# Performance work log

Hardware: AMD Instinct MI355X
Metric: run time of the kernel (lower is better)

Reference implementation:

```python
import math
import jax, jax.numpy as jnp
import numpy as np

B, T, D = 8, 2048, 512


def setup_inputs() -> dict:
    key = jax.random.key(0)
    kx, = jax.random.split(key, 1)
    x = jax.random.normal(kx, (B, T, D), dtype=jnp.float32)
    log_tau = jnp.asarray(math.log(2.0), dtype=jnp.float32)
    log_blend = jnp.asarray(math.log(0.3 / 0.7), dtype=jnp.float32)
    return {"x": x, "log_tau": log_tau, "log_blend": log_blend}


def _gelu_tanh(x):
    c = math.sqrt(2.0 / math.pi)
    return 0.5 * x * (1.0 + jnp.tanh(c * (x + 0.044715 * x * x * x)))


def reference(x, log_tau, log_blend):
    Bb, Tt, Dd = x.shape
    tau = jnp.exp(log_tau)
    alpha = jax.nn.sigmoid(log_blend)
    # F.normalize(x, dim=-1): divide by L2 norm clamped to eps=1e-12
    norm = jnp.maximum(jnp.linalg.norm(x, axis=-1, keepdims=True), 1e-12)
    x_norm = x / norm
    # cosine self-similarity [B, T, T]
    sim = jnp.einsum("btd,bsd->bts", x_norm, x_norm)
    # triu(diagonal=0) masks j >= i (current + future positions)
    causal_mask = jnp.triu(jnp.ones((Tt, Tt), dtype=bool), k=0)
    sim_causal = jnp.where(causal_mask[None, :, :], -jnp.inf, sim)
    max_sim = jnp.max(sim_causal, axis=-1)  # [B, T]; row 0 is -inf
    max_sim = jnp.nan_to_num(max_sim, nan=0.0, posinf=1.0, neginf=-1.0)
    novelty = jnp.exp(-tau * max_sim)
    scale = (1.0 - alpha + alpha * novelty)[..., None]  # [B, T, 1]
    return _gelu_tanh(x * scale)
```

## Files before the change

kernel.cpp:

```cpp
#include <hip/hip_runtime.h>

#define B_ 8
#define T_ 2048
#define D_ 512
#define BT 128
#define BK 64
#define NT (T_/BT)
#define NTILES (NT*(NT+1)/2)
#define KTILES (D_/BK)

typedef float f32x4 __attribute__((ext_vector_type(4)));
typedef __bf16 bf16x8 __attribute__((ext_vector_type(8)));

__device__ __forceinline__ unsigned encf(float f) {
    int i = __float_as_int(f);
    return (i < 0) ? ~((unsigned)i) : (((unsigned)i) | 0x80000000u);
}
__device__ __forceinline__ float decf(unsigned u) {
    unsigned b = (u & 0x80000000u) ? (u ^ 0x80000000u) : ~u;
    return __int_as_float((int)b);
}

__device__ __forceinline__ void gload_lds16(const __bf16* g, __bf16* l) {
    __builtin_amdgcn_global_load_lds(
        (const __attribute__((address_space(1))) unsigned int*)g,
        (__attribute__((address_space(3))) unsigned int*)l, 16, 0, 0);
}

__global__ __launch_bounds__(256) void rownorm_kernel(
        const float* __restrict__ x, __bf16* __restrict__ xn,
        unsigned* __restrict__ msim) {
    int row  = blockIdx.x * 4 + (threadIdx.x >> 6);
    int lane = threadIdx.x & 63;
    const float* p = x + (size_t)row * D_ + lane * 8;
    float4 a = *(const float4*)p;
    float4 b = *(const float4*)(p + 4);
    float ss = a.x*a.x + a.y*a.y + a.z*a.z + a.w*a.w
             + b.x*b.x + b.y*b.y + b.z*b.z + b.w*b.w;
#pragma unroll
    for (int m = 32; m; m >>= 1) ss += __shfl_xor(ss, m);
    float r = 1.0f / fmaxf(sqrtf(ss), 1e-12f);
    bf16x8 h;
    h[0] = (__bf16)(a.x * r); h[1] = (__bf16)(a.y * r);
    h[2] = (__bf16)(a.z * r); h[3] = (__bf16)(a.w * r);
    h[4] = (__bf16)(b.x * r); h[5] = (__bf16)(b.y * r);
    h[6] = (__bf16)(b.z * r); h[7] = (__bf16)(b.w * r);
    *(bf16x8*)(xn + (size_t)row * D_ + lane * 8) = h;
    if (lane == 0) msim[row] = 0x407FFFFFu;
}

__global__ __launch_bounds__(256, 2) void simmax_kernel(
        const __bf16* __restrict__ xn, unsigned* __restrict__ msim) {
    __shared__ __attribute__((aligned(16))) __bf16 sA[2][BT * BK];
    __shared__ __attribute__((aligned(16))) __bf16 sB[2][BT * BK];

    int bid = blockIdx.x;
    int b   = bid & 7;
    int s   = bid >> 3;
    int it  = 0;
    while ((it + 1) * (it + 2) / 2 <= s) it++;
    int jt  = s - it * (it + 1) / 2;
    const bool diag = (it == jt);

    int tid  = threadIdx.x;
    int lane = tid & 63;
    int w    = tid >> 6;
    int wr   = w >> 1;
    int wc   = w & 1;
    int fr   = lane & 15;
    int kg   = lane >> 4;

    const size_t rowA0 = (size_t)b * T_ + (size_t)it * BT;
    const size_t rowB0 = (size_t)b * T_ + (size_t)jt * BT;

    int rb   = lane >> 3;
    int csrc = (lane & 7) ^ rb;
    const __bf16* gA = xn + (rowA0 + w * 8 + rb) * D_ + csrc * 8;
    const __bf16* gB = xn + (rowB0 + w * 8 + rb) * D_ + csrc * 8;

    f32x4 acc[4][4];
#pragma unroll
    for (int m = 0; m < 4; m++)
#pragma unroll
        for (int n = 0; n < 4; n++)
            acc[m][n] = (f32x4){0.f, 0.f, 0.f, 0.f};

    int swz = (fr & 7) << 4;
    int laA = (wr * 64 + fr) * 128 + kg * 16;
    int laB = (wc * 64 + fr) * 128 + kg * 16;

#define STAGE_A(buf, kc) do {                                              \
    _Pragma("unroll")                                                      \
    for (int p = 0; p < 4; p++)                                            \
        gload_lds16(gA + (size_t)p * 32 * D_ + (kc) * BK,                  \
                    &sA[buf][(p * 32 + w * 8) * BK]);                      \
} while (0)
#define STAGE_B(buf, kc) do {                                              \
    _Pragma("unroll")                                                      \
    for (int p = 0; p < 4; p++)                                            \
        gload_lds16(gB + (size_t)p * 32 * D_ + (kc) * BK,                  \
                    &sB[buf][(p * 32 + w * 8) * BK]);                      \
} while (0)

    STAGE_A(0, 0);
    if (!diag) STAGE_B(0, 0);

    for (int kc = 0; kc < KTILES; kc++) {
        int cur = kc & 1, nxt = cur ^ 1;
        if (kc < KTILES - 1) {
            STAGE_A(nxt, kc + 1);
            asm volatile("s_waitcnt vmcnt(4)" ::: "memory");
        } else {
            asm volatile("s_waitcnt vmcnt(0)" ::: "memory");
        }
        __builtin_amdgcn_sched_barrier(0);
        asm volatile("s_barrier" ::: "memory");
        __builtin_amdgcn_sched_barrier(0);

        const char* bA = (const char*)&sA[cur][0];
        const char* bB = diag ? (const char*)&sA[cur][0]
                              : (const char*)&sB[cur][0];

        bf16x8 af[4][2], b0[2][2];
#pragma unroll
        for (int m = 0; m < 4; m++)
#pragma unroll
            for (int ks = 0; ks < 2; ks++)
                af[m][ks] = *(const bf16x8*)(bA +
                              ((laA + m * 2048 + ks * 64) ^ swz));
#pragma unroll
        for (int n = 0; n < 2; n++)
#pragma unroll
            for (int ks = 0; ks < 2; ks++)
                b0[n][ks] = *(const bf16x8*)(bB +
                              ((laB + n * 2048 + ks * 64) ^ swz));
        asm volatile("s_waitcnt lgkmcnt(0)" ::: "memory");
        __builtin_amdgcn_sched_barrier(0);
        __builtin_amdgcn_s_setprio(1);
#pragma unroll
        for (int m = 0; m < 4; m++)
#pragma unroll
            for (int n = 0; n < 2; n++)
#pragma unroll
                for (int ks = 0; ks < 2; ks++)
                    acc[m][n] = __builtin_amdgcn_mfma_f32_16x16x32_bf16(
                        af[m][ks], b0[n][ks], acc[m][n], 0, 0, 0);
        __builtin_amdgcn_s_setprio(0);
        __builtin_amdgcn_sched_barrier(0);

        if (kc < KTILES - 1 && !diag) STAGE_B(nxt, kc + 1);

        bf16x8 b1[2][2];
#pragma unroll
        for (int n = 0; n < 2; n++)
#pragma unroll
            for (int ks = 0; ks < 2; ks++)
                b1[n][ks] = *(const bf16x8*)(bB +
                              ((laB + (n + 2) * 2048 + ks * 64) ^ swz));
        asm volatile("s_waitcnt lgkmcnt(0)" ::: "memory");
        __builtin_amdgcn_sched_barrier(0);
        __builtin_amdgcn_s_setprio(1);
#pragma unroll
        for (int m = 0; m < 4; m++)
#pragma unroll
            for (int n = 0; n < 2; n++)
#pragma unroll
                for (int ks = 0; ks < 2; ks++)
                    acc[m][n + 2] = __builtin_amdgcn_mfma_f32_16x16x32_bf16(
                        af[m][ks], b1[n][ks], acc[m][n + 2], 0, 0, 0);
        __builtin_amdgcn_s_setprio(0);
        __builtin_amdgcn_sched_barrier(0);
    }
#undef STAGE_A
#undef STAGE_B

    unsigned* mrow = msim + (size_t)b * T_ + (size_t)it * BT;
    const float NINF = -__builtin_inff();
#pragma unroll
    for (int m = 0; m < 4; m++) {
#pragma unroll
        for (int e = 0; e < 4; e++) {
            int rloc = wr * 64 + m * 16 + kg * 4 + e;
            float v = NINF;
#pragma unroll
            for (int n = 0; n < 4; n++) {
                int cloc = wc * 64 + n * 16 + fr;
                float t = acc[m][n][e];
                if (diag && cloc >= rloc) t = NINF;
                v = fmaxf(v, t);
            }
            v = fmaxf(v, __shfl_xor(v, 1));
            v = fmaxf(v, __shfl_xor(v, 2));
            v = fmaxf(v, __shfl_xor(v, 4));
            v = fmaxf(v, __shfl_xor(v, 8));
            if (fr == 0) atomicMax(&mrow[rloc], encf(v));
        }
    }
}

__global__ __launch_bounds__(256) void gelu_kernel(
        const float* __restrict__ x, const unsigned* __restrict__ msim,
        const float* __restrict__ ltau, const float* __restrict__ lblend,
        float* __restrict__ out) {
    int i = blockIdx.x * 256 + threadIdx.x;
    float tau   = __expf(ltau[0]);
    float alpha = 1.f / (1.f + __expf(-lblend[0]));
    int row = i >> 7;
    float ms = decf(msim[row]);
    float sc = (1.f - alpha) + alpha * __expf(-tau * ms);
    float4 v = ((const float4*)x)[i];
    const float c0 = 0.7978845608028654f;
    const float c1 = 0.044715f;
    float4 o;
#pragma unroll
    for (int j = 0; j < 4; j++) {
        float z = ((const float*)&v)[j] * sc;
        float u = c0 * (z + c1 * z * z * z);
        float t = __expf(2.f * u);
        float th = 1.f - 2.f / (t + 1.f);
        ((float*)&o)[j] = 0.5f * z * (1.f + th);
    }
    ((float4*)out)[i] = o;
}

extern "C" void kernel_launch(void* const* d_in, const int* in_sizes, int n_in,
                              void* d_out, int out_size, void* d_ws, size_t ws_size,
                              hipStream_t stream) {
    (void)in_sizes; (void)n_in; (void)out_size; (void)ws_size;
    const float* x      = (const float*)d_in[0];
    const float* ltau   = (const float*)d_in[1];
    const float* lblend = (const float*)d_in[2];
    float*    out   = (float*)d_out;
    __bf16*   xn    = (__bf16*)d_out;
    unsigned* msim  = (unsigned*)d_ws;

    rownorm_kernel<<<B_ * T_ / 4, 256, 0, stream>>>(x, xn, msim);
    simmax_kernel<<<B_ * NTILES, 256, 0, stream>>>(xn, msim);
    gelu_kernel<<<(B_ * T_ * D_ / 4) / 256, 256, 0, stream>>>(x, msim, ltau, lblend, out);
}
```

Baseline: 63.35 us.

## Use 256x256 off-diagonal tiles with 512-thread blocks and small diagonal tiles

The causal similarity-max kernel now covers strictly-lower off-diagonal 256x256 blocks with 8-wave, 512-thread workgroups, and handles the diagonal band with 128x128 tiles (two diagonal and one sub-diagonal per 256 block). Larger tiles double the arithmetic intensity per LDS/global load and cut the number of workgroups and atomics. The K loop is also reworked to prefetch two stages ahead. The cost is more accumulator registers per thread (128 floats), which may limit occupancy, plus an uneven workload mix between big and small blocks.

New measurement: 57.31 us. 1.11x faster.

```diff
diff --git a/kernel.cpp b/kernel.cpp
--- a/kernel.cpp
+++ b/kernel.cpp
@@ -3,11 +3,10 @@
 #define B_ 8
 #define T_ 2048
 #define D_ 512
-#define BT 128
 #define BK 64
-#define NT (T_/BT)
-#define NTILES (NT*(NT+1)/2)
-#define KTILES (D_/BK)
+#define KT 8
+#define NBIG 28
+#define NSMALL 24
 
 typedef float f32x4 __attribute__((ext_vector_type(4)));
 typedef __bf16 bf16x8 __attribute__((ext_vector_type(8)));
@@ -49,151 +48,269 @@
     if (lane == 0) msim[row] = 0x407FFFFFu;
 }
 
-__global__ __launch_bounds__(256, 2) void simmax_kernel(
+__global__ __launch_bounds__(512, 2) void simmax_kernel(
         const __bf16* __restrict__ xn, unsigned* __restrict__ msim) {
-    __shared__ __attribute__((aligned(16))) __bf16 sA[2][BT * BK];
-    __shared__ __attribute__((aligned(16))) __bf16 sB[2][BT * BK];
-
-    int bid = blockIdx.x;
-    int b   = bid & 7;
-    int s   = bid >> 3;
-    int it  = 0;
-    while ((it + 1) * (it + 2) / 2 <= s) it++;
-    int jt  = s - it * (it + 1) / 2;
-    const bool diag = (it == jt);
+    __shared__ __attribute__((aligned(16))) __bf16 sA[2][2][128 * BK];
+    __shared__ __attribute__((aligned(16))) __bf16 sB[2][2][128 * BK];
+
+    int bid  = blockIdx.x;
+    int b    = bid & 7;
+    int u    = bid >> 3;
 
     int tid  = threadIdx.x;
     int lane = tid & 63;
     int w    = tid >> 6;
-    int wr   = w >> 1;
-    int wc   = w & 1;
+    int wr   = w >> 2;
+    int wc   = w & 3;
     int fr   = lane & 15;
     int kg   = lane >> 4;
-
-    const size_t rowA0 = (size_t)b * T_ + (size_t)it * BT;
-    const size_t rowB0 = (size_t)b * T_ + (size_t)jt * BT;
-
     int rb   = lane >> 3;
     int csrc = (lane & 7) ^ rb;
-    const __bf16* gA = xn + (rowA0 + w * 8 + rb) * D_ + csrc * 8;
-    const __bf16* gB = xn + (rowB0 + w * 8 + rb) * D_ + csrc * 8;
-
-    f32x4 acc[4][4];
-#pragma unroll
-    for (int m = 0; m < 4; m++)
-#pragma unroll
-        for (int n = 0; n < 4; n++)
-            acc[m][n] = (f32x4){0.f, 0.f, 0.f, 0.f};
-
-    int swz = (fr & 7) << 4;
-    int laA = (wr * 64 + fr) * 128 + kg * 16;
-    int laB = (wc * 64 + fr) * 128 + kg * 16;
-
-#define STAGE_A(buf, kc) do {                                              \
-    _Pragma("unroll")                                                      \
-    for (int p = 0; p < 4; p++)                                            \
-        gload_lds16(gA + (size_t)p * 32 * D_ + (kc) * BK,                  \
-                    &sA[buf][(p * 32 + w * 8) * BK]);                      \
-} while (0)
-#define STAGE_B(buf, kc) do {                                              \
-    _Pragma("unroll")                                                      \
-    for (int p = 0; p < 4; p++)                                            \
-        gload_lds16(gB + (size_t)p * 32 * D_ + (kc) * BK,                  \
-                    &sB[buf][(p * 32 + w * 8) * BK]);                      \
-} while (0)
-
-    STAGE_A(0, 0);
-    if (!diag) STAGE_B(0, 0);
-
-    for (int kc = 0; kc < KTILES; kc++) {
-        int cur = kc & 1, nxt = cur ^ 1;
-        if (kc < KTILES - 1) {
-            STAGE_A(nxt, kc + 1);
-            asm volatile("s_waitcnt vmcnt(4)" ::: "memory");
-        } else {
-            asm volatile("s_waitcnt vmcnt(0)" ::: "memory");
-        }
+    int swz  = (fr & 7) << 4;
+    const float NINF = -__builtin_inff();
+
+    if (u < NBIG) {
+        int it = 1; while (it * (it + 1) / 2 <= u) it++;
+        int jt = u - it * (it - 1) / 2;
+        const size_t rowA0 = (size_t)b * T_ + (size_t)it * 256;
+        const size_t rowB0 = (size_t)b * T_ + (size_t)jt * 256;
+        const __bf16* gA = xn + (rowA0 + w * 16 + rb) * D_ + csrc * 8;
+        const __bf16* gB = xn + (rowB0 + w * 16 + rb) * D_ + csrc * 8;
+
+#define STAGEB(s, kc) do {                                                  \
+    _Pragma("unroll")                                                       \
+    for (int h = 0; h < 2; h++)                                             \
+    _Pragma("unroll")                                                       \
+    for (int q = 0; q < 2; q++) {                                           \
+        gload_lds16(gA + ((size_t)h * 128 + q * 8) * D_ + (kc) * BK,        \
+                    &sA[s][h][(w * 16 + q * 8) * BK]);                      \
+        gload_lds16(gB + ((size_t)h * 128 + q * 8) * D_ + (kc) * BK,        \
+                    &sB[s][h][(w * 16 + q * 8) * BK]);                      \
+    } } while (0)
+
+        f32x4 acc[8][4];
+#pragma unroll
+        for (int m = 0; m < 8; m++)
+#pragma unroll
+            for (int n = 0; n < 4; n++)
+                acc[m][n] = (f32x4){0.f, 0.f, 0.f, 0.f};
+
+        STAGEB(0, 0);
+        STAGEB(1, 1);
+        asm volatile("s_waitcnt vmcnt(8)" ::: "memory");
         __builtin_amdgcn_sched_barrier(0);
         asm volatile("s_barrier" ::: "memory");
+
+        int laA = fr * 128 + kg * 16;
+        int laB = ((wc & 1) * 64 + fr) * 128 + kg * 16;
+
+        for (int kt = 0; kt < KT; kt++) {
+            int s = kt & 1;
+            const char* bA = (const char*)&sA[s][wr][0];
+            const char* bB = (const char*)&sB[s][wc >> 1][0];
+
+            bf16x8 af[8][2], bf[2][2];
+#pragma unroll
+            for (int m = 0; m < 4; m++)
+#pragma unroll
+                for (int ks = 0; ks < 2; ks++)
+                    af[m][ks] = *(const bf16x8*)(bA + ((laA + m * 2048 + ks * 64) ^ swz));
+#pragma unroll
+            for (int n = 0; n < 2; n++)
+#pragma unroll
+                for (int ks = 0; ks < 2; ks++)
+                    bf[n][ks] = *(const bf16x8*)(bB + ((laB + n * 2048 + ks * 64) ^ swz));
+            asm volatile("s_waitcnt lgkmcnt(0)" ::: "memory");
+            __builtin_amdgcn_sched_barrier(0);
+            __builtin_amdgcn_s_setprio(1);
+#pragma unroll
+            for (int m = 0; m < 4; m++)
+#pragma unroll
+                for (int n = 0; n < 2; n++)
+#pragma unroll
+                    for (int ks = 0; ks < 2; ks++)
+                        acc[m][n] = __builtin_amdgcn_mfma_f32_16x16x32_bf16(
+                            af[m][ks], bf[n][ks], acc[m][n], 0, 0, 0);
+            __builtin_amdgcn_s_setprio(0);
+            __builtin_amdgcn_sched_barrier(0);
+
+#pragma unroll
+            for (int m = 4; m < 8; m++)
+#pragma unroll
+                for (int ks = 0; ks < 2; ks++)
+                    af[m][ks] = *(const bf16x8*)(bA + ((laA + m * 2048 + ks * 64) ^ swz));
+            asm volatile("s_waitcnt lgkmcnt(0)" ::: "memory");
+            __builtin_amdgcn_sched_barrier(0);
+            __builtin_amdgcn_s_setprio(1);
+#pragma unroll
+            for (int m = 4; m < 8; m++)
+#pragma unroll
+                for (int n = 0; n < 2; n++)
+#pragma unroll
+                    for (int ks = 0; ks < 2; ks++)
+                        acc[m][n] = __builtin_amdgcn_mfma_f32_16x16x32_bf16(
+                            af[m][ks], bf[n][ks], acc[m][n], 0, 0, 0);
+            __builtin_amdgcn_s_setprio(0);
+            __builtin_amdgcn_sched_barrier(0);
+
+#pragma unroll
+            for (int n = 0; n < 2; n++)
+#pragma unroll
+                for (int ks = 0; ks < 2; ks++)
+                    bf[n][ks] = *(const bf16x8*)(bB + ((laB + (n + 2) * 2048 + ks * 64) ^ swz));
+            asm volatile("s_waitcnt lgkmcnt(0)" ::: "memory");
+            __builtin_amdgcn_sched_barrier(0);
+            __builtin_amdgcn_s_setprio(1);
+#pragma unroll
+            for (int m = 0; m < 4; m++)
+#pragma unroll
+                for (int n = 0; n < 2; n++)
+#pragma unroll
+                    for (int ks = 0; ks < 2; ks++)
+                        acc[m][n + 2] = __builtin_amdgcn_mfma_f32_16x16x32_bf16(
+                            af[m][ks], bf[n][ks], acc[m][n + 2], 0, 0, 0);
+            __builtin_amdgcn_s_setprio(0);
+            __builtin_amdgcn_sched_barrier(0);
+
+            __builtin_amdgcn_s_setprio(1);
+#pragma unroll
+            for (int m = 4; m < 8; m++)
+#pragma unroll
+                for (int n = 0; n < 2; n++)
+#pragma unroll
+                    for (int ks = 0; ks < 2; ks++)
+                        acc[m][n + 2] = __builtin_amdgcn_mfma_f32_16x16x32_bf16(
+                            af[m][ks], bf[n][ks], acc[m][n + 2], 0, 0, 0);
+            __builtin_amdgcn_s_setprio(0);
+            __builtin_amdgcn_sched_barrier(0);
+
+            if (kt == KT - 1) break;
+            asm volatile("s_barrier" ::: "memory");
+            if (kt + 2 < KT) {
+                STAGEB(s, kt + 2);
+                asm volatile("s_waitcnt vmcnt(8)" ::: "memory");
+            } else {
+                asm volatile("s_waitcnt vmcnt(0)" ::: "memory");
+            }
+            __builtin_amdgcn_sched_barrier(0);
+            asm volatile("s_barrier" ::: "memory");
+        }
+#undef STAGEB
+
+        unsigned* mrow = msim + rowA0;
+#pragma unroll
+        for (int m = 0; m < 8; m++) {
+#pragma unroll
+            for (int e = 0; e < 4; e++) {
+                int rloc = wr * 128 + m * 16 + kg * 4 + e;
+                float v = NINF;
+#pragma unroll
+                for (int n = 0; n < 4; n++) v = fmaxf(v, acc[m][n][e]);
+                v = fmaxf(v, __shfl_xor(v, 1));
+                v = fmaxf(v, __shfl_xor(v, 2));
+                v = fmaxf(v, __shfl_xor(v, 4));
+                v = fmaxf(v, __shfl_xor(v, 8));
+                if (fr == 0) atomicMax(&mrow[rloc], encf(v));
+            }
+        }
+    } else {
+        int u2 = u - NBIG;
+        int d  = u2 / 3, r = u2 - 3 * d;
+        int it = 2 * d + (r >= 1 ? 1 : 0);
+        int jt = 2 * d + (r == 2 ? 1 : 0);
+        const bool diag = (r != 1);
+        const size_t rowA0 = (size_t)b * T_ + (size_t)it * 128;
+        const size_t rowB0 = (size_t)b * T_ + (size_t)jt * 128;
+        const __bf16* gA = xn + (rowA0 + w * 16 + rb) * D_ + csrc * 8;
+        const __bf16* gB = xn + (rowB0 + w * 16 + rb) * D_ + csrc * 8;
+
+#define STAGES(s, kc) do {                                                  \
+    _Pragma("unroll")                                                       \
+    for (int q = 0; q < 2; q++) {                                           \
+        gload_lds16(gA + (size_t)q * 8 * D_ + (kc) * BK,                    \
+                    &sA[s][0][(w * 16 + q * 8) * BK]);                      \
+        gload_lds16(gB + (size_t)q * 8 * D_ + (kc) * BK,                    \
+                    &sB[s][0][(w * 16 + q * 8) * BK]);                      \
+    } } while (0)
+
+        f32x4 acc[4][2];
+#pragma unroll
+        for (int m = 0; m < 4; m++)
+#pragma unroll
+            for (int n = 0; n < 2; n++)
+                acc[m][n] = (f32x4){0.f, 0.f, 0.f, 0.f};
+
+        STAGES(0, 0);
+        STAGES(1, 1);
+        asm volatile("s_waitcnt vmcnt(4)" ::: "memory");
         __builtin_amdgcn_sched_barrier(0);
-
-        const char* bA = (const char*)&sA[cur][0];
-        const char* bB = diag ? (const char*)&sA[cur][0]
-                              : (const char*)&sB[cur][0];
-
-        bf16x8 af[4][2], b0[2][2];
-#pragma unroll
-        for (int m = 0; m < 4; m++)
-#pragma unroll
-            for (int ks = 0; ks < 2; ks++)
-                af[m][ks] = *(const bf16x8*)(bA +
-                              ((laA + m * 2048 + ks * 64) ^ swz));
-#pragma unroll
-        for (int n = 0; n < 2; n++)
-#pragma unroll
-            for (int ks = 0; ks < 2; ks++)
-                b0[n][ks] = *(const bf16x8*)(bB +
-                              ((laB + n * 2048 + ks * 64) ^ swz));
-        asm volatile("s_waitcnt lgkmcnt(0)" ::: "memory");
-        __builtin_amdgcn_sched_barrier(0);
-        __builtin_amdgcn_s_setprio(1);
-#pragma unroll
-        for (int m = 0; m < 4; m++)
+        asm volatile("s_barrier" ::: "memory");
+
+        int laA = (wr * 64 + fr) * 128 + kg * 16;
+        int laB = (wc * 32 + fr) * 128 + kg * 16;
+
+        for (int kt = 0; kt < KT; kt++) {
+            int s = kt & 1;
+            const char* bA = (const char*)&sA[s][0][0];
+            const char* bB = (const char*)&sB[s][0][0];
+            bf16x8 af[4][2], bf[2][2];
+#pragma unroll
+            for (int m = 0; m < 4; m++)
+#pragma unroll
+                for (int ks = 0; ks < 2; ks++)
+                    af[m][ks] = *(const bf16x8*)(bA + ((laA + m * 2048 + ks * 64) ^ swz));
 #pragma unroll
             for (int n = 0; n < 2; n++)
 #pragma unroll
                 for (int ks = 0; ks < 2; ks++)
-                    acc[m][n] = __builtin_amdgcn_mfma_f32_16x16x32_bf16(
-                        af[m][ks], b0[n][ks], acc[m][n], 0, 0, 0);
-        __builtin_amdgcn_s_setprio(0);
-        __builtin_amdgcn_sched_barrier(0);
-
-        if (kc < KTILES - 1 && !diag) STAGE_B(nxt, kc + 1);
-
-        bf16x8 b1[2][2];
-#pragma unroll
-        for (int n = 0; n < 2; n++)
-#pragma unroll
-            for (int ks = 0; ks < 2; ks++)
-                b1[n][ks] = *(const bf16x8*)(bB +
-                              ((laB + (n + 2) * 2048 + ks * 64) ^ swz));
-        asm volatile("s_waitcnt lgkmcnt(0)" ::: "memory");
-        __builtin_amdgcn_sched_barrier(0);
-        __builtin_amdgcn_s_setprio(1);
-#pragma unroll
-        for (int m = 0; m < 4; m++)
-#pragma unroll
-            for (int n = 0; n < 2; n++)
-#pragma unroll
-                for (int ks = 0; ks < 2; ks++)
-                    acc[m][n + 2] = __builtin_amdgcn_mfma_f32_16x16x32_bf16(
-                        af[m][ks], b1[n][ks], acc[m][n + 2], 0, 0, 0);
-        __builtin_amdgcn_s_setprio(0);
-        __builtin_amdgcn_sched_barrier(0);
-    }
-#undef STAGE_A
-#undef STAGE_B
-
-    unsigned* mrow = msim + (size_t)b * T_ + (size_t)it * BT;
-    const float NINF = -__builtin_inff();
-#pragma unroll
-    for (int m = 0; m < 4; m++) {
-#pragma unroll
-        for (int e = 0; e < 4; e++) {
-            int rloc = wr * 64 + m * 16 + kg * 4 + e;
-            float v = NINF;
-#pragma unroll
-            for (int n = 0; n < 4; n++) {
-                int cloc = wc * 64 + n * 16 + fr;
-                float t = acc[m][n][e];
-                if (diag && cloc >= rloc) t = NINF;
-                v = fmaxf(v, t);
+                    bf[n][ks] = *(const bf16x8*)(bB + ((laB + n * 2048 + ks * 64) ^ swz));
+            asm volatile("s_waitcnt lgkmcnt(0)" ::: "memory");
+            __builtin_amdgcn_sched_barrier(0);
+            __builtin_amdgcn_s_setprio(1);
+#pragma unroll
+            for (int m = 0; m < 4; m++)
+#pragma unroll
+                for (int n = 0; n < 2; n++)
+#pragma unroll
+                    for (int ks = 0; ks < 2; ks++)
+                        acc[m][n] = __builtin_amdgcn_mfma_f32_16x16x32_bf16(
+                            af[m][ks], bf[n][ks], acc[m][n], 0, 0, 0);
+            __builtin_amdgcn_s_setprio(0);
+            __builtin_amdgcn_sched_barrier(0);
+
+            if (kt == KT - 1) break;
+            asm volatile("s_barrier" ::: "memory");
+            if (kt + 2 < KT) {
+                STAGES(s, kt + 2);
+                asm volatile("s_waitcnt vmcnt(4)" ::: "memory");
+            } else {
+                asm volatile("s_waitcnt vmcnt(0)" ::: "memory");
             }
-            v = fmaxf(v, __shfl_xor(v, 1));
-            v = fmaxf(v, __shfl_xor(v, 2));
-            v = fmaxf(v, __shfl_xor(v, 4));
-            v = fmaxf(v, __shfl_xor(v, 8));
-            if (fr == 0) atomicMax(&mrow[rloc], encf(v));
+            __builtin_amdgcn_sched_barrier(0);
+            asm volatile("s_barrier" ::: "memory");
+        }
+#undef STAGES
+
+        unsigned* mrow = msim + rowA0;
+#pragma unroll
+        for (int m = 0; m < 4; m++) {
+#pragma unroll
+            for (int e = 0; e < 4; e++) {
+                int rloc = wr * 64 + m * 16 + kg * 4 + e;
+                float v = NINF;
+#pragma unroll
+                for (int n = 0; n < 2; n++) {
+                    int cloc = wc * 32 + n * 16 + fr;
+                    float t = acc[m][n][e];
+                    if (diag && cloc >= rloc) t = NINF;
+                    v = fmaxf(v, t);
+                }
+                v = fmaxf(v, __shfl_xor(v, 1));
+                v = fmaxf(v, __shfl_xor(v, 2));
+                v = fmaxf(v, __shfl_xor(v, 4));
+                v = fmaxf(v, __shfl_xor(v, 8));
+                if (fr == 0) atomicMax(&mrow[rloc], encf(v));
+            }
         }
     }
 }
@@ -215,8 +332,8 @@
 #pragma unroll
     for (int j = 0; j < 4; j++) {
         float z = ((const float*)&v)[j] * sc;
-        float u = c0 * (z + c1 * z * z * z);
-        float t = __expf(2.f * u);
+        float uu = c0 * (z + c1 * z * z * z);
+        float t = __expf(2.f * uu);
         float th = 1.f - 2.f / (t + 1.f);
         ((float*)&o)[j] = 0.5f * z * (1.f + th);
     }
@@ -235,6 +352,6 @@
     unsigned* msim  = (unsigned*)d_ws;
 
     rownorm_kernel<<<B_ * T_ / 4, 256, 0, stream>>>(x, xn, msim);
-    simmax_kernel<<<B_ * NTILES, 256, 0, stream>>>(xn, msim);
+    simmax_kernel<<<B_ * (NBIG + NSMALL), 512, 0, stream>>>(xn, msim);
     gelu_kernel<<<(B_ * T_ * D_ / 4) / 256, 256, 0, stream>>>(x, msim, ltau, lblend, out);
 }
```
